# Optimization experiments

Measured on AMD Instinct MI355X. Metric: run time of the kernel, lower is better.

## Reference

```python
import jax, jax.numpy as jnp
import numpy as np

N, S, E, HEADS = 8, 2048, 1024, 16


def setup_inputs() -> dict:
    root = jax.random.key(0)
    k1, k2, k3, k4, k5, k6 = jax.random.split(root, 6)
    query = jax.random.normal(k1, (N, S, E), jnp.float32)
    key_t = jax.random.normal(k2, (N, S, E), jnp.float32)
    value = jax.random.normal(k3, (N, S, E), jnp.float32)
    # mask broadcasts against the (buggy) energy tensor of shape (N, S, H, H)
    mask = jax.random.randint(k4, (1, 1, HEADS, HEADS), 0, 2, jnp.int32)
    # guarantee no all-masked softmax row (avoid NaN)
    diag = jnp.arange(HEADS)
    mask = mask.at[0, 0, diag, diag].set(1)
    W_out = jax.random.normal(k5, (E, E), jnp.float32) / np.float32(np.sqrt(E))
    b_out = jax.random.normal(k6, (E,), jnp.float32) * 0.02
    return {"query": query, "key": key_t, "value": value, "mask": mask,
            "W_out": W_out, "b_out": b_out, "heads": HEADS}


def reference(query, key, value, mask, W_out, b_out, heads):
    # Faithful translation of the original forward, INCLUDING its einsum-label
    # bug: tensors are transposed to (N, H, S, D) but the einsum subscripts
    # treat axis 1 as 'q/k' and axis 2 as 'h', so softmax runs over heads.
    n, q_len, e = query.shape
    d = e // heads
    inv_scale = np.float32(1.0 / np.sqrt(d))
    q = query.reshape(n, q_len, heads, d).transpose(0, 2, 1, 3)   # (N,H,S,D)
    k = key.reshape(n, q_len, heads, d).transpose(0, 2, 1, 3)     # (N,H,S,D)
    v = value.reshape(n, q_len, heads, d).transpose(0, 2, 1, 3)   # (N,H,S,D)
    # labels applied to transposed tensors -> energy shape (N, S, H, H)
    energy = jnp.einsum('nqhd,nkhd->nhqk', q, k) * inv_scale
    energy = jnp.where(mask == 0, -jnp.inf, energy)
    attention = jax.nn.softmax(energy, axis=-1)                   # over heads axis
    out = jnp.einsum('nhql,nlhd->nqhd', attention, v)             # (N,H,S,D)
    out = out.reshape(n, q_len, e)                                # raw memory reinterp, as torch does
    return out @ W_out.T + b_out
```

## Files before the change

### kernel.cpp

```cpp
#include <hip/hip_runtime.h>
#include <stdint.h>

#define S_LEN 2048
#define EMB 1024

typedef __bf16 bf16x8 __attribute__((ext_vector_type(8)));
typedef __bf16 bf16x4 __attribute__((ext_vector_type(4)));
typedef float f32x4 __attribute__((ext_vector_type(4)));

__device__ __forceinline__ unsigned short f2bf(float f) {
  unsigned int b = __float_as_uint(f);
  b += 0x7FFFu + ((b >> 16) & 1u);
  return (unsigned short)(b >> 16);
}

__device__ __forceinline__ bf16x8 cvt8(float4 a, float4 b) {
  bf16x8 r;
  r[0] = (__bf16)a.x; r[1] = (__bf16)a.y; r[2] = (__bf16)a.z; r[3] = (__bf16)a.w;
  r[4] = (__bf16)b.x; r[5] = (__bf16)b.y; r[6] = (__bf16)b.z; r[7] = (__bf16)b.w;
  return r;
}

#define GLD16(gp, lp)                                                          \
  __builtin_amdgcn_global_load_lds(                                            \
      (const __attribute__((address_space(1))) void*)(gp),                     \
      (__attribute__((address_space(3))) void*)(lp), 16, 0, 0)

__device__ __forceinline__ float4 lds_rd4(const float* base, int byteoff) {
  const int sw = byteoff ^ (((byteoff >> 8) & 7) << 5);
  return *(const float4*)((const char*)base + sw);
}

__global__ __launch_bounds__(256) void attn_kernel(
    const float* __restrict__ Q, const float* __restrict__ K,
    const float* __restrict__ V, const int* __restrict__ mask,
    __bf16* __restrict__ X) {
  __shared__ float Qf[2][2][1024];
  __shared__ float Kf[2][2][1024];
  __shared__ float Vf[2][2][1024];
  __shared__ __bf16 As[2][16][16];

  const int t = threadIdx.x;
  const int lane = t & 63;
  const int wv = t >> 6;
  const int pos0 = blockIdx.x * 16;
  const int n = pos0 >> 11;
  const int col = lane & 15;
  const int grp = lane >> 4;
  const int gc = grp & 1;

  const int L = t * 16;
  const int Lsw = L ^ (((L >> 8) & 7) << 5);

  const int4 mrow = *(const int4*)(mask + col * 16 + grp * 4);

  auto STAGE = [&](int buf, int step) {
#pragma unroll
    for (int pp = 0; pp < 2; ++pp) {
      const int pos = pos0 + step * 2 + pp;
      const char* qsrc = (const char*)(Q + (size_t)pos * EMB);
      const char* ksrc = (const char*)(K + (size_t)pos * EMB);
      const char* vsrc = (const char*)(V + (size_t)pos * EMB);
      GLD16(qsrc + Lsw, (char*)&Qf[buf][pp][0] + L);
      GLD16(ksrc + Lsw, (char*)&Kf[buf][pp][0] + L);
      GLD16(vsrc + L, (char*)&Vf[buf][pp][0] + L);
    }
  };

  auto COMPUTE = [&](int buf, int step) {
    if (wv >= 2) return;
    const int pos = pos0 + step * 2 + wv;
    const int s = pos & 2047;
    const float* qf = &Qf[buf][wv][0];
    const float* kf = &Kf[buf][wv][0];
    const float* vf4 = &Vf[buf][wv][0];

    const int R0 = col * 256 + grp * 32;
    const bf16x8 qa0 = cvt8(lds_rd4(qf, R0), lds_rd4(qf, R0 + 16));
    const bf16x8 qa1 = cvt8(lds_rd4(qf, R0 + 128), lds_rd4(qf, R0 + 144));
    const bf16x8 kb0 = cvt8(lds_rd4(kf, R0), lds_rd4(kf, R0 + 16));
    const bf16x8 kb1 = cvt8(lds_rd4(kf, R0 + 128), lds_rd4(kf, R0 + 144));

    f32x4 en = {0.f, 0.f, 0.f, 0.f};
    en = __builtin_amdgcn_mfma_f32_16x16x32_bf16(kb0, qa0, en, 0, 0, 0);
    en = __builtin_amdgcn_mfma_f32_16x16x32_bf16(kb1, qa1, en, 0, 0, 0);

    float p[4];
    p[0] = (mrow.x == 0) ? -1e30f : en[0] * 0.125f;
    p[1] = (mrow.y == 0) ? -1e30f : en[1] * 0.125f;
    p[2] = (mrow.z == 0) ? -1e30f : en[2] * 0.125f;
    p[3] = (mrow.w == 0) ? -1e30f : en[3] * 0.125f;
    float mx = fmaxf(fmaxf(p[0], p[1]), fmaxf(p[2], p[3]));
    mx = fmaxf(mx, __shfl_xor(mx, 16));
    mx = fmaxf(mx, __shfl_xor(mx, 32));
    float ex[4], sm = 0.f;
#pragma unroll
    for (int r = 0; r < 4; ++r) {
      ex[r] = __expf(p[r] - mx);
      sm += ex[r];
    }
    sm += __shfl_xor(sm, 16);
    sm += __shfl_xor(sm, 32);
    const float inv = __builtin_amdgcn_rcpf(sm);
    bf16x4 aw;
#pragma unroll
    for (int r = 0; r < 4; ++r) aw[r] = (__bf16)(ex[r] * inv);
    *(bf16x4*)&As[wv][col][grp * 4] = aw;

    const bf16x8 pt = *(const bf16x8*)&As[wv][col][gc * 8];
    bf16x8 pa;
#pragma unroll
    for (int e = 0; e < 8; ++e) pa[e] = (grp < 2) ? pt[e] : (__bf16)0.f;

    const size_t xrow = (size_t)n * S_LEN + (size_t)col * 128 + (s >> 4);
    __bf16* xp = X + xrow * EMB + (size_t)((s & 15) * 64 + grp * 4);
#pragma unroll
    for (int c = 0; c < 4; ++c) {
      bf16x8 vf;
#pragma unroll
      for (int e = 0; e < 8; ++e)
        vf[e] = (__bf16)vf4[(gc * 8 + e) * 64 + c * 16 + col];
      f32x4 o = {0.f, 0.f, 0.f, 0.f};
      o = __builtin_amdgcn_mfma_f32_16x16x32_bf16(vf, pa, o, 0, 0, 0);
      bf16x4 w;
#pragma unroll
      for (int r = 0; r < 4; ++r) w[r] = (__bf16)o[r];
      *(bf16x4*)(xp + c * 16) = w;
    }
  };

  STAGE(0, 0);
  __syncthreads();
#pragma unroll 2
  for (int step = 0; step < 8; ++step) {
    if (step + 1 < 8) STAGE((step + 1) & 1, step + 1);
    COMPUTE(step & 1, step);
    __syncthreads();
  }
}

__global__ __launch_bounds__(256) void wconv_kernel(
    const float* __restrict__ W, unsigned short* __restrict__ Wb) {
  const int idx = blockIdx.x * 256 + threadIdx.x;
  float4 w = *(const float4*)(W + (size_t)idx * 4);
  ushort4 o;
  o.x = f2bf(w.x);
  o.y = f2bf(w.y);
  o.z = f2bf(w.z);
  o.w = f2bf(w.w);
  *(ushort4*)(Wb + (size_t)idx * 4) = o;
}

__global__ __launch_bounds__(256) void gemm_kernel(
    const unsigned short* __restrict__ A, const unsigned short* __restrict__ B,
    const float* __restrict__ bias, float* __restrict__ C) {
  __shared__ unsigned short sA[128 * 32];
  __shared__ unsigned short sB[128 * 32];

  int bid = blockIdx.x;
  const int cpx = gridDim.x >> 3;
  bid = (bid & 7) * cpx + (bid >> 3);
  const int tileM = (bid >> 3) * 128;
  const int tileN = (bid & 7) * 128;

  const int t = threadIdx.x;
  const int lane = t & 63;
  const int wid = t >> 6;
  const int wm = wid >> 1, wn = wid & 1;
  const int lrow = lane & 15;
  const int lgrp = lane >> 4;

  f32x4 acc[4][4];
#pragma unroll
  for (int a = 0; a < 4; ++a)
#pragma unroll
    for (int b = 0; b < 4; ++b) acc[a][b] = (f32x4){0.f, 0.f, 0.f, 0.f};

  const int row0 = t >> 2;
  const int kk = (t & 3) * 8;
  const size_t abase = ((size_t)(tileM + row0)) * 1024 + kk;
  const size_t bbase = ((size_t)(tileN + row0)) * 1024 + kk;

  for (int k0 = 0; k0 < 1024; k0 += 32) {
#pragma unroll
    for (int c = 0; c < 2; ++c) {
      GLD16(A + abase + (size_t)c * 64 * 1024 + k0,
            (char*)sA + c * 4096 + t * 16);
      GLD16(B + bbase + (size_t)c * 64 * 1024 + k0,
            (char*)sB + c * 4096 + t * 16);
    }
    __syncthreads();

    bf16x8 af[4], bfr[4];
#pragma unroll
    for (int mi = 0; mi < 4; ++mi)
      af[mi] = *(const bf16x8*)&sA[(wm * 64 + mi * 16 + lrow) * 32 + lgrp * 8];
#pragma unroll
    for (int ni = 0; ni < 4; ++ni)
      bfr[ni] = *(const bf16x8*)&sB[(wn * 64 + ni * 16 + lrow) * 32 + lgrp * 8];
#pragma unroll
    for (int mi = 0; mi < 4; ++mi)
#pragma unroll
      for (int ni = 0; ni < 4; ++ni)
        acc[mi][ni] = __builtin_amdgcn_mfma_f32_16x16x32_bf16(
            af[mi], bfr[ni], acc[mi][ni], 0, 0, 0);
    __syncthreads();
  }

#pragma unroll
  for (int ni = 0; ni < 4; ++ni) {
    const int colc = tileN + wn * 64 + ni * 16 + lrow;
    const float bv = bias[colc];
#pragma unroll
    for (int mi = 0; mi < 4; ++mi) {
      const int row = tileM + wm * 64 + mi * 16 + lgrp * 4;
#pragma unroll
      for (int r = 0; r < 4; ++r)
        C[(size_t)(row + r) * 1024 + colc] = acc[mi][ni][r] + bv;
    }
  }
}

extern "C" void kernel_launch(void* const* d_in, const int* in_sizes, int n_in,
                              void* d_out, int out_size, void* d_ws,
                              size_t ws_size, hipStream_t stream) {
  const float* Q = (const float*)d_in[0];
  const float* K = (const float*)d_in[1];
  const float* V = (const float*)d_in[2];
  const int* mask = (const int*)d_in[3];
  const float* W = (const float*)d_in[4];
  const float* bias = (const float*)d_in[5];
  float* out = (float*)d_out;

  __bf16* X = (__bf16*)d_ws;
  unsigned short* Wb =
      (unsigned short*)((char*)d_ws + (size_t)32 * 1024 * 1024);

  hipLaunchKernelGGL(attn_kernel, dim3(8 * S_LEN / 16), dim3(256), 0, stream,
                     Q, K, V, mask, X);
  hipLaunchKernelGGL(wconv_kernel, dim3(1024), dim3(256), 0, stream, W, Wb);
  hipLaunchKernelGGL(gemm_kernel, dim3(1024), dim3(256), 0, stream,
                     (const unsigned short*)X, Wb, bias, out);
}
```

Baseline: 107.0 us.

## Stage attention inputs as bf16 in LDS via register prefetch, use all four waves

The attention kernel stops using direct global-to-LDS fp32 copies. Each thread now loads float4s into registers, converts them to bf16 and writes them to swizzled LDS, with the next step's global loads issued before the current compute to keep the double buffer. All four waves now compute one position each per step instead of only two, so there are four steps instead of eight, and LDS holds half-size bf16 data. The aim is to raise wave utilisation and shrink LDS traffic and conversions, at the cost of more registers held across the compute for the prefetched data.

Measured after the change: 99.29 us, median of 2. 7.2% less time.

```diff
diff --git a/kernel.cpp b/kernel.cpp
--- a/kernel.cpp
+++ b/kernel.cpp
@@ -14,10 +14,9 @@
   return (unsigned short)(b >> 16);
 }
 
-__device__ __forceinline__ bf16x8 cvt8(float4 a, float4 b) {
-  bf16x8 r;
+__device__ __forceinline__ bf16x4 c4(float4 a) {
+  bf16x4 r;
   r[0] = (__bf16)a.x; r[1] = (__bf16)a.y; r[2] = (__bf16)a.z; r[3] = (__bf16)a.w;
-  r[4] = (__bf16)b.x; r[5] = (__bf16)b.y; r[6] = (__bf16)b.z; r[7] = (__bf16)b.w;
   return r;
 }
 
@@ -26,19 +25,18 @@
       (const __attribute__((address_space(1))) void*)(gp),                     \
       (__attribute__((address_space(3))) void*)(lp), 16, 0, 0)
 
-__device__ __forceinline__ float4 lds_rd4(const float* base, int byteoff) {
-  const int sw = byteoff ^ (((byteoff >> 8) & 7) << 5);
-  return *(const float4*)((const char*)base + sw);
+__device__ __forceinline__ int swz(int L) {
+  return L ^ (((L >> 7) & 7) << 4);
 }
 
 __global__ __launch_bounds__(256) void attn_kernel(
     const float* __restrict__ Q, const float* __restrict__ K,
     const float* __restrict__ V, const int* __restrict__ mask,
     __bf16* __restrict__ X) {
-  __shared__ float Qf[2][2][1024];
-  __shared__ float Kf[2][2][1024];
-  __shared__ float Vf[2][2][1024];
-  __shared__ __bf16 As[2][16][16];
+  __shared__ __bf16 Qb[2][4][1024];
+  __shared__ __bf16 Kb[2][4][1024];
+  __shared__ __bf16 Vb[2][4][1024];
+  __shared__ __bf16 As[4][16][16];
 
   const int t = threadIdx.x;
   const int lane = t & 63;
@@ -49,37 +47,44 @@
   const int grp = lane >> 4;
   const int gc = grp & 1;
 
-  const int L = t * 16;
-  const int Lsw = L ^ (((L >> 8) & 7) << 5);
-
   const int4 mrow = *(const int4*)(mask + col * 16 + grp * 4);
 
-  auto STAGE = [&](int buf, int step) {
-#pragma unroll
-    for (int pp = 0; pp < 2; ++pp) {
-      const int pos = pos0 + step * 2 + pp;
-      const char* qsrc = (const char*)(Q + (size_t)pos * EMB);
-      const char* ksrc = (const char*)(K + (size_t)pos * EMB);
-      const char* vsrc = (const char*)(V + (size_t)pos * EMB);
-      GLD16(qsrc + Lsw, (char*)&Qf[buf][pp][0] + L);
-      GLD16(ksrc + Lsw, (char*)&Kf[buf][pp][0] + L);
-      GLD16(vsrc + L, (char*)&Vf[buf][pp][0] + L);
+  const int Lw = 8 * t;
+  const int LwS = swz(Lw);
+
+  float4 fq[4], fk[4], fv[4];
+
+  auto ISSUE = [&](int step) {
+#pragma unroll
+    for (int p = 0; p < 4; ++p) {
+      const size_t base = (size_t)(pos0 + step * 4 + p) * EMB + t * 4;
+      fq[p] = *(const float4*)(Q + base);
+      fk[p] = *(const float4*)(K + base);
+      fv[p] = *(const float4*)(V + base);
     }
   };
+  auto WRITE = [&](int buf) {
+#pragma unroll
+    for (int p = 0; p < 4; ++p) {
+      *(bf16x4*)((char*)&Qb[buf][p][0] + LwS) = c4(fq[p]);
+      *(bf16x4*)((char*)&Kb[buf][p][0] + LwS) = c4(fk[p]);
+      *(bf16x4*)((char*)&Vb[buf][p][0] + Lw) = c4(fv[p]);
+    }
+  };
 
   auto COMPUTE = [&](int buf, int step) {
-    if (wv >= 2) return;
-    const int pos = pos0 + step * 2 + wv;
+    const int pos = pos0 + step * 4 + wv;
     const int s = pos & 2047;
-    const float* qf = &Qf[buf][wv][0];
-    const float* kf = &Kf[buf][wv][0];
-    const float* vf4 = &Vf[buf][wv][0];
-
-    const int R0 = col * 256 + grp * 32;
-    const bf16x8 qa0 = cvt8(lds_rd4(qf, R0), lds_rd4(qf, R0 + 16));
-    const bf16x8 qa1 = cvt8(lds_rd4(qf, R0 + 128), lds_rd4(qf, R0 + 144));
-    const bf16x8 kb0 = cvt8(lds_rd4(kf, R0), lds_rd4(kf, R0 + 16));
-    const bf16x8 kb1 = cvt8(lds_rd4(kf, R0 + 128), lds_rd4(kf, R0 + 144));
+    const __bf16* qr = &Qb[buf][wv][0];
+    const __bf16* kr = &Kb[buf][wv][0];
+    const __bf16* vr = &Vb[buf][wv][0];
+
+    const int L0 = col * 128 + grp * 16;
+    const int L1 = L0 + 64;
+    const bf16x8 qa0 = *(const bf16x8*)((const char*)qr + swz(L0));
+    const bf16x8 qa1 = *(const bf16x8*)((const char*)qr + swz(L1));
+    const bf16x8 kb0 = *(const bf16x8*)((const char*)kr + swz(L0));
+    const bf16x8 kb1 = *(const bf16x8*)((const char*)kr + swz(L1));
 
     f32x4 en = {0.f, 0.f, 0.f, 0.f};
     en = __builtin_amdgcn_mfma_f32_16x16x32_bf16(kb0, qa0, en, 0, 0, 0);
@@ -119,7 +124,7 @@
       bf16x8 vf;
 #pragma unroll
       for (int e = 0; e < 8; ++e)
-        vf[e] = (__bf16)vf4[(gc * 8 + e) * 64 + c * 16 + col];
+        vf[e] = vr[(gc * 8 + e) * 64 + c * 16 + col];
       f32x4 o = {0.f, 0.f, 0.f, 0.f};
       o = __builtin_amdgcn_mfma_f32_16x16x32_bf16(vf, pa, o, 0, 0, 0);
       bf16x4 w;
@@ -129,12 +134,18 @@
     }
   };
 
-  STAGE(0, 0);
+  ISSUE(0);
+  WRITE(0);
   __syncthreads();
-#pragma unroll 2
-  for (int step = 0; step < 8; ++step) {
-    if (step + 1 < 8) STAGE((step + 1) & 1, step + 1);
-    COMPUTE(step & 1, step);
+#pragma unroll
+  for (int step = 0; step < 4; ++step) {
+    const int buf = step & 1;
+    if (step < 3) {
+      ISSUE(step + 1);
+      __builtin_amdgcn_sched_barrier(0);
+    }
+    COMPUTE(buf, step);
+    if (step < 3) WRITE(buf ^ 1);
     __syncthreads();
   }
 }
```
